# Kernel optimization log

Measured on AMD Instinct MI355X. Metric: run time of the kernel, lower is better.

## Reference

```python
import jax, jax.numpy as jnp
import numpy as np

B, S, P, D, H = 2, 4096, 1024, 1024, 16  # batch, byte seq, patches, d_model, heads


def setup_inputs() -> dict:
    key = jax.random.key(0)
    ks = jax.random.split(key, 8)
    init = 0.02
    queries = jax.random.normal(ks[0], (B, S, D), dtype=jnp.float32)
    patch_representations = jax.random.normal(ks[1], (B, P, D), dtype=jnp.float32)
    patch_boundaries = jax.random.randint(ks[2], (B, S), 0, 2, dtype=jnp.int32)
    wq = jax.random.normal(ks[3], (D, D), dtype=jnp.float32) * init
    wk = jax.random.normal(ks[4], (D, D), dtype=jnp.float32) * init
    wv = jax.random.normal(ks[5], (D, D), dtype=jnp.float32) * init
    wo = jax.random.normal(ks[6], (D, D), dtype=jnp.float32) * init
    bq = jnp.zeros((D,), jnp.float32)
    bk = jnp.zeros((D,), jnp.float32)
    bv = jnp.zeros((D,), jnp.float32)
    bo = jnp.zeros((D,), jnp.float32)
    return {"queries": queries, "patch_representations": patch_representations,
            "patch_boundaries": patch_boundaries,
            "wq": wq, "wk": wk, "wv": wv, "wo": wo,
            "bq": bq, "bk": bk, "bv": bv, "bo": bo}


def reference(queries, patch_representations, patch_boundaries,
              wq, wk, wv, wo, bq, bk, bv, bo):
    b, s, d = queries.shape
    p = patch_representations.shape[1]
    h = H
    dh = d // h
    scale = 1.0 / jnp.sqrt(jnp.asarray(dh, queries.dtype))

    # in-projections (torch Linear: x @ W.T + b)
    q = (queries @ wq.T + bq).reshape(b, s, h, dh)
    k = (patch_representations @ wk.T + bk).reshape(b, p, h, dh)
    v = (patch_representations @ wv.T + bv).reshape(b, p, h, dh)

    # scores: [b, h, s, p]
    scores = jnp.einsum('bqhd,bkhd->bhqk', q, k) * scale

    # data-dependent patch-boundary mask: byte t may attend to patch j iff j <= cumsum(boundaries)[t]
    patch_idx = jnp.cumsum(patch_boundaries, axis=1)          # [b, s]
    mask = jnp.arange(p)[None, None, :] > patch_idx[:, :, None]  # [b, s, p], True = masked
    scores = jnp.where(mask[:, None, :, :], jnp.finfo(scores.dtype).min, scores)

    attn = jax.nn.softmax(scores, axis=-1)                    # dropout inactive (eval)
    out = jnp.einsum('bhqk,bkhd->bqhd', attn, v).reshape(b, s, d)
    return out @ wo.T + bo
```

## Files before the change

kernel.cpp:

```cpp
#include <hip/hip_runtime.h>


#define B_ 2
#define S_ 4096
#define P_ 1024
#define D_ 1024
#define H_ 16
#define DH_ 64

#define NCONV 14336

typedef __attribute__((ext_vector_type(8))) short short8;
typedef __attribute__((ext_vector_type(4))) float f32x4;

#define KSCALE 0.18033688011112042f

static __device__ __forceinline__ unsigned short f2bf(float f) {
    unsigned int u = __float_as_uint(f);
    u += 0x7FFFu + ((u >> 16) & 1u);
    return (unsigned short)(u >> 16);
}

static __device__ __forceinline__ void gll16(const unsigned short* g,
                                             const unsigned short* l) {
    __builtin_amdgcn_global_load_lds(
        (const __attribute__((address_space(1))) unsigned int*)g,
        (__attribute__((address_space(3))) unsigned int*)l,
        16, 0, 0);
}

__global__ __launch_bounds__(256) void xattn_convert_all(
    const float* __restrict__ queries, const float* __restrict__ patches,
    const float* __restrict__ wq, const float* __restrict__ wk,
    const float* __restrict__ wv, const float* __restrict__ wo,
    unsigned short* __restrict__ qb, unsigned short* __restrict__ pb,
    unsigned short* __restrict__ wqb, unsigned short* __restrict__ wkb,
    unsigned short* __restrict__ wvb, unsigned short* __restrict__ wob,
    const int* __restrict__ bounds, int* __restrict__ pidx) {
    if (blockIdx.x >= NCONV) {
        __shared__ int sdata[256];
        int b = blockIdx.x - NCONV;
        int t = threadIdx.x;
        const int* src = bounds + b * S_ + t * 16;
        int vals[16];
        int run = 0;
#pragma unroll
        for (int i = 0; i < 16; ++i) { run += src[i]; vals[i] = run; }
        sdata[t] = run;
        __syncthreads();
        for (int off = 1; off < 256; off <<= 1) {
            int v = (t >= off) ? sdata[t - off] : 0;
            __syncthreads();
            sdata[t] += v;
            __syncthreads();
        }
        int prefix = (t > 0) ? sdata[t - 1] : 0;
        int* dst = pidx + b * S_ + t * 16;
#pragma unroll
        for (int i = 0; i < 16; ++i) dst[i] = prefix + vals[i];
        return;
    }
    const int NQ = (B_ * S_ * D_) / 4;
    const int NP = (B_ * P_ * D_) / 4;
    const int NW = (D_ * D_) / 4;
    int i = blockIdx.x * 256 + threadIdx.x;
    const float* src;
    unsigned short* dst;
    int j;
    if (i < NQ) { src = queries; dst = qb; j = i; }
    else if (i < NQ + NP) { src = patches; dst = pb; j = i - NQ; }
    else {
        int k = i - NQ - NP;
        int wsel = k >> 18;
        j = k & (NW - 1);
        if (wsel == 0) { src = wq; dst = wqb; }
        else if (wsel == 1) { src = wk; dst = wkb; }
        else if (wsel == 2) { src = wv; dst = wvb; }
        else { src = wo; dst = wob; }
    }
    float4 v = ((const float4*)src)[j];
    ushort4 o;
    o.x = f2bf(v.x); o.y = f2bf(v.y); o.z = f2bf(v.z); o.w = f2bf(v.w);
    ((ushort4*)dst)[j] = o;
}

__global__ __launch_bounds__(256) void xattn_gemm_qkv(
    const unsigned short* __restrict__ qb, const unsigned short* __restrict__ pb,
    const unsigned short* __restrict__ wqb, const unsigned short* __restrict__ wkb,
    const unsigned short* __restrict__ wvb,
    const float* __restrict__ bq, const float* __restrict__ bk,
    const float* __restrict__ bv,
    unsigned short* __restrict__ Qout, unsigned short* __restrict__ Kout,
    unsigned short* __restrict__ Vout) {
    const int K = 1024, N = 1024;
    const int z = blockIdx.z;
    if (z > 0 && blockIdx.y >= 16) return;
    const unsigned short* A = (z == 0) ? qb : pb;
    const unsigned short* W = (z == 0) ? wqb : ((z == 1) ? wkb : wvb);
    const float* bias = (z == 0) ? bq : ((z == 1) ? bk : bv);

    __shared__ unsigned short As[128 * 32];
    __shared__ unsigned short Bs[128 * 32];

    const int m0 = blockIdx.y * 128;
    const int n0 = blockIdx.x * 128;
    const int t = threadIdx.x;
    const int w = t >> 6;
    const int l = t & 63;
    const int fr = l & 15, fq = l >> 4;
    const int wr = w >> 1, wc = w & 1;

    const int r0s = t >> 2;
    const int cs = (t & 3) * 8;
    const unsigned short* Ap0 = A + (size_t)(m0 + r0s) * K + cs;
    const unsigned short* Ap1 = A + (size_t)(m0 + 64 + r0s) * K + cs;
    const unsigned short* Wp0 = W + (size_t)(n0 + r0s) * K + cs;
    const unsigned short* Wp1 = W + (size_t)(n0 + 64 + r0s) * K + cs;
    const unsigned short* lA0 = &As[(w * 64) * 8];
    const unsigned short* lA1 = &As[(256 + w * 64) * 8];
    const unsigned short* lB0 = &Bs[(w * 64) * 8];
    const unsigned short* lB1 = &Bs[(256 + w * 64) * 8];

    f32x4 acc[4][4];
#pragma unroll
    for (int i = 0; i < 4; ++i)
#pragma unroll
        for (int j = 0; j < 4; ++j) acc[i][j] = (f32x4){0.f, 0.f, 0.f, 0.f};

    for (int k0 = 0; k0 < K; k0 += 32) {
        gll16(Ap0 + k0, lA0);
        gll16(Ap1 + k0, lA1);
        gll16(Wp0 + k0, lB0);
        gll16(Wp1 + k0, lB1);
        __syncthreads();
        short8 af[4], bf[4];
#pragma unroll
        for (int i = 0; i < 4; ++i)
            af[i] = *(const short8*)&As[(wr * 64 + i * 16 + fr) * 32 + fq * 8];
#pragma unroll
        for (int j = 0; j < 4; ++j)
            bf[j] = *(const short8*)&Bs[(wc * 64 + j * 16 + fr) * 32 + fq * 8];
#pragma unroll
        for (int i = 0; i < 4; ++i)
#pragma unroll
            for (int j = 0; j < 4; ++j)
                acc[i][j] = __builtin_amdgcn_mfma_f32_16x16x32_bf16(af[i], bf[j], acc[i][j], 0, 0, 0);
        __syncthreads();
    }

#pragma unroll
    for (int j = 0; j < 4; ++j) {
        int n = n0 + wc * 64 + j * 16 + fr;
        float bvv = bias[n];
#pragma unroll
        for (int i = 0; i < 4; ++i) {
            int mbase = m0 + wr * 64 + i * 16 + fq * 4;
#pragma unroll
            for (int r = 0; r < 4; ++r) {
                float val = acc[i][j][r] + bvv;
                int m = mbase + r;
                if (z == 0) {
                    Qout[(size_t)m * N + n] = f2bf(val * KSCALE);
                } else if (z == 1) {
                    Kout[(size_t)m * N + n] = f2bf(val);
                } else {
                    int bb = m >> 10, c = m & (P_ - 1);
                    int hh = n >> 6, d = n & 63;
                    Vout[(((size_t)(bb * H_ + hh)) * 64 + d) * P_ + c] = f2bf(val);
                }
            }
        }
    }
}

__global__ __launch_bounds__(256) void xattn_gemm_o(
    const unsigned short* __restrict__ A,
    const unsigned short* __restrict__ W,
    const float* __restrict__ bias,
    float* __restrict__ Cout) {
    const int K = 1024, N = 1024;
    __shared__ unsigned short As[128 * 32];
    __shared__ unsigned short Bs[128 * 32];

    const int m0 = blockIdx.y * 128;
    const int n0 = blockIdx.x * 128;
    const int t = threadIdx.x;
    const int w = t >> 6;
    const int l = t & 63;
    const int fr = l & 15, fq = l >> 4;
    const int wr = w >> 1, wc = w & 1;

    const int r0s = t >> 2;
    const int cs = (t & 3) * 8;
    const unsigned short* Ap0 = A + (size_t)(m0 + r0s) * K + cs;
    const unsigned short* Ap1 = A + (size_t)(m0 + 64 + r0s) * K + cs;
    const unsigned short* Wp0 = W + (size_t)(n0 + r0s) * K + cs;
    const unsigned short* Wp1 = W + (size_t)(n0 + 64 + r0s) * K + cs;
    const unsigned short* lA0 = &As[(w * 64) * 8];
    const unsigned short* lA1 = &As[(256 + w * 64) * 8];
    const unsigned short* lB0 = &Bs[(w * 64) * 8];
    const unsigned short* lB1 = &Bs[(256 + w * 64) * 8];

    f32x4 acc[4][4];
#pragma unroll
    for (int i = 0; i < 4; ++i)
#pragma unroll
        for (int j = 0; j < 4; ++j) acc[i][j] = (f32x4){0.f, 0.f, 0.f, 0.f};

    for (int k0 = 0; k0 < K; k0 += 32) {
        gll16(Ap0 + k0, lA0);
        gll16(Ap1 + k0, lA1);
        gll16(Wp0 + k0, lB0);
        gll16(Wp1 + k0, lB1);
        __syncthreads();
        short8 af[4], bf[4];
#pragma unroll
        for (int i = 0; i < 4; ++i)
            af[i] = *(const short8*)&As[(wr * 64 + i * 16 + fr) * 32 + fq * 8];
#pragma unroll
        for (int j = 0; j < 4; ++j)
            bf[j] = *(const short8*)&Bs[(wc * 64 + j * 16 + fr) * 32 + fq * 8];
#pragma unroll
        for (int i = 0; i < 4; ++i)
#pragma unroll
            for (int j = 0; j < 4; ++j)
                acc[i][j] = __builtin_amdgcn_mfma_f32_16x16x32_bf16(af[i], bf[j], acc[i][j], 0, 0, 0);
        __syncthreads();
    }

#pragma unroll
    for (int j = 0; j < 4; ++j) {
        int n = n0 + wc * 64 + j * 16 + fr;
        float bvv = bias[n];
#pragma unroll
        for (int i = 0; i < 4; ++i) {
            int mbase = m0 + wr * 64 + i * 16 + fq * 4;
#pragma unroll
            for (int r = 0; r < 4; ++r)
                Cout[(size_t)(mbase + r) * N + n] = acc[i][j][r] + bvv;
        }
    }
}

__global__ __launch_bounds__(256) void xattn_attn_mfma(
    const unsigned short* __restrict__ Qb,
    const unsigned short* __restrict__ Kb,
    const unsigned short* __restrict__ Vtb,
    const int* __restrict__ pidx,
    unsigned short* __restrict__ Ob) {
    __shared__ unsigned short Ks[64 * 72];
    __shared__ unsigned short Vs[64 * 72];
    __shared__ unsigned short Ps[64 * 72];

    const int q0 = (63 - blockIdx.x) * 64;
    const int h = blockIdx.y;
    const int b = blockIdx.z;
    const int t = threadIdx.x;
    const int w = t >> 6, l = t & 63;
    const int fr = l & 15, fq = l >> 4;

    const unsigned short* qrow =
        Qb + (size_t)(b * S_ + q0 + w * 16 + fr) * D_ + h * DH_ + fq * 8;
    short8 qf0 = *(const short8*)qrow;
    short8 qf1 = *(const short8*)(qrow + 32);

    int prow[4];
#pragma unroll
    for (int r = 0; r < 4; ++r)
        prow[r] = pidx[b * S_ + q0 + w * 16 + fq * 4 + r];
    const int limit = pidx[b * S_ + q0 + 63];
    const int ntiles = (min(limit, P_ - 1) + 64) >> 6;
    const int nfull = (pidx[b * S_ + q0] + 1) >> 6;

    float lsum[4] = {0.f, 0.f, 0.f, 0.f};
    f32x4 oacc[4];
#pragma unroll
    for (int nt = 0; nt < 4; ++nt) oacc[nt] = (f32x4){0.f, 0.f, 0.f, 0.f};

    const int srow = t >> 3, sseg = t & 7;
    const unsigned short* kbase = Kb + (size_t)(b * P_) * D_ + h * DH_;
    const unsigned short* vbase = Vtb + (size_t)(b * H_ + h) * 64 * P_;
    unsigned short* ksa = &Ks[srow * 72 + sseg * 8];
    unsigned short* ksb = &Ks[(srow + 32) * 72 + sseg * 8];
    unsigned short* vsa = &Vs[srow * 72 + sseg * 8];
    unsigned short* vsb = &Vs[(srow + 32) * 72 + sseg * 8];

    uint4 rk0 = *(const uint4*)(kbase + (size_t)srow * D_ + sseg * 8);
    uint4 rk1 = *(const uint4*)(kbase + (size_t)(srow + 32) * D_ + sseg * 8);
    uint4 rv0 = *(const uint4*)(vbase + (size_t)srow * P_ + sseg * 8);
    uint4 rv1 = *(const uint4*)(vbase + (size_t)(srow + 32) * P_ + sseg * 8);
    *(uint4*)ksa = rk0;
    *(uint4*)ksb = rk1;
    *(uint4*)vsa = rv0;
    *(uint4*)vsb = rv1;
    __syncthreads();

    for (int kt = 0; kt < ntiles; ++kt) {
        const int c0 = kt * 64;
        const int c0n = min(c0 + 64, P_ - 64);
        rk0 = *(const uint4*)(kbase + (size_t)(c0n + srow) * D_ + sseg * 8);
        rk1 = *(const uint4*)(kbase + (size_t)(c0n + srow + 32) * D_ + sseg * 8);
        rv0 = *(const uint4*)(vbase + (size_t)srow * P_ + c0n + sseg * 8);
        rv1 = *(const uint4*)(vbase + (size_t)(srow + 32) * P_ + c0n + sseg * 8);

        const int maskme = (kt >= nfull);
#pragma unroll
        for (int nt = 0; nt < 4; ++nt) {
            short8 kf0 = *(const short8*)&Ks[(nt * 16 + fr) * 72 + fq * 8];
            short8 kf1 = *(const short8*)&Ks[(nt * 16 + fr) * 72 + 32 + fq * 8];
            const int col = c0 + nt * 16 + fr;
            f32x4 a = (f32x4){0.f, 0.f, 0.f, 0.f};
            a = __builtin_amdgcn_mfma_f32_16x16x32_bf16(qf0, kf0, a, 0, 0, 0);
            a = __builtin_amdgcn_mfma_f32_16x16x32_bf16(qf1, kf1, a, 0, 0, 0);
#pragma unroll
            for (int r = 0; r < 4; ++r) {
                float p = exp2f(a[r]);
                if (maskme) p = (col > prow[r]) ? 0.f : p;
                lsum[r] += p;
                Ps[(w * 16 + fq * 4 + r) * 72 + nt * 16 + fr] = f2bf(p);
            }
        }
        short8 pf0 = *(const short8*)&Ps[(w * 16 + fr) * 72 + fq * 8];
        short8 pf1 = *(const short8*)&Ps[(w * 16 + fr) * 72 + 32 + fq * 8];
#pragma unroll
        for (int nt = 0; nt < 4; ++nt) {
            short8 vf0 = *(const short8*)&Vs[(nt * 16 + fr) * 72 + fq * 8];
            short8 vf1 = *(const short8*)&Vs[(nt * 16 + fr) * 72 + 32 + fq * 8];
            oacc[nt] = __builtin_amdgcn_mfma_f32_16x16x32_bf16(pf0, vf0, oacc[nt], 0, 0, 0);
            oacc[nt] = __builtin_amdgcn_mfma_f32_16x16x32_bf16(pf1, vf1, oacc[nt], 0, 0, 0);
        }
        __syncthreads();
        *(uint4*)ksa = rk0;
        *(uint4*)ksb = rk1;
        *(uint4*)vsa = rv0;
        *(uint4*)vsb = rv1;
        __syncthreads();
    }

#pragma unroll
    for (int off = 1; off < 16; off <<= 1) {
#pragma unroll
        for (int r = 0; r < 4; ++r)
            lsum[r] += __shfl_xor(lsum[r], off);
    }
    float inv[4];
#pragma unroll
    for (int r = 0; r < 4; ++r) inv[r] = 1.0f / lsum[r];

    unsigned short* obase = Ob + (size_t)(b * S_ + q0 + w * 16) * D_ + h * DH_;
#pragma unroll
    for (int nt = 0; nt < 4; ++nt)
#pragma unroll
        for (int r = 0; r < 4; ++r)
            obase[(size_t)(fq * 4 + r) * D_ + nt * 16 + fr] =
                f2bf(oacc[nt][r] * inv[r]);
}

extern "C" void kernel_launch(void* const* d_in, const int* in_sizes, int n_in,
                              void* d_out, int out_size, void* d_ws, size_t ws_size,
                              hipStream_t stream) {
    const float* queries = (const float*)d_in[0];
    const float* patches = (const float*)d_in[1];
    const int* bounds    = (const int*)d_in[2];
    const float* wq = (const float*)d_in[3];
    const float* wk = (const float*)d_in[4];
    const float* wv = (const float*)d_in[5];
    const float* wo = (const float*)d_in[6];
    const float* bq = (const float*)d_in[7];
    const float* bk = (const float*)d_in[8];
    const float* bv = (const float*)d_in[9];
    const float* bo = (const float*)d_in[10];
    float* out = (float*)d_out;

    char* ws = (char*)d_ws;
    unsigned short* qb    = (unsigned short*)(ws + 0);
    unsigned short* pb    = (unsigned short*)(ws + 16777216);
    unsigned short* wqb   = (unsigned short*)(ws + 20971520);
    unsigned short* wkb   = (unsigned short*)(ws + 23068672);
    unsigned short* wvb   = (unsigned short*)(ws + 25165824);
    unsigned short* wob   = (unsigned short*)(ws + 27262976);
    unsigned short* Qbf   = (unsigned short*)(ws + 29360128);
    unsigned short* Kbf   = (unsigned short*)(ws + 46137344);
    unsigned short* Vtb   = (unsigned short*)(ws + 50331648);
    unsigned short* attnb = (unsigned short*)(ws + 54525952);
    int* pidx             = (int*)(ws + 71303168);

    xattn_convert_all<<<dim3(NCONV + B_), 256, 0, stream>>>(
        queries, patches, wq, wk, wv, wo, qb, pb, wqb, wkb, wvb, wob,
        bounds, pidx);
    xattn_gemm_qkv<<<dim3(8, 64, 3), 256, 0, stream>>>(
        qb, pb, wqb, wkb, wvb, bq, bk, bv, Qbf, Kbf, Vtb);
    xattn_attn_mfma<<<dim3(S_ / 64, H_, B_), 256, 0, stream>>>(
        Qbf, Kbf, Vtb, pidx, attnb);
    xattn_gemm_o<<<dim3(8, 64), 256, 0, stream>>>(attnb, wob, bo, out);
}
```

Baseline: 266.9 us.

## Permute V columns, pack P tile with perm stores, use fast exp2, drop register prefetch

The V projection epilogue now writes V columns in a permuted order within each 64-wide chunk. This lets the attention kernel store probabilities with packed 8-byte writes (built with byte-perm truncation to bf16) instead of sixteen scalar rounded stores. The exp2 call becomes the hardware builtin, and the masked and unmasked tiles use separate loops. The register double-buffered K/V prefetch is removed in favour of a plain load-then-sync per tile, which lowers register pressure but exposes global load latency. The packed store also truncates to bf16 instead of rounding.

```diff
diff --git a/kernel.cpp b/kernel.cpp
--- a/kernel.cpp
+++ b/kernel.cpp
@@ -14,6 +14,12 @@
 typedef __attribute__((ext_vector_type(4))) float f32x4;
 
 #define KSCALE 0.18033688011112042f
+
+#if __has_builtin(__builtin_amdgcn_exp2f)
+#define EXP2(x) __builtin_amdgcn_exp2f(x)
+#else
+#define EXP2(x) exp2f(x)
+#endif
 
 static __device__ __forceinline__ unsigned short f2bf(float f) {
     unsigned int u = __float_as_uint(f);
@@ -166,7 +172,9 @@
                 } else {
                     int bb = m >> 10, c = m & (P_ - 1);
                     int hh = n >> 6, d = n & 63;
-                    Vout[(((size_t)(bb * H_ + hh)) * 64 + d) * P_ + c] = f2bf(val);
+                    int cl = c & 63;
+                    int cp = (c & 960) | (((cl & 15) << 2) | (cl >> 4));
+                    Vout[(((size_t)(bb * H_ + hh)) * 64 + d) * P_ + cp] = f2bf(val);
                 }
             }
         }
@@ -280,45 +288,62 @@
     const int srow = t >> 3, sseg = t & 7;
     const unsigned short* kbase = Kb + (size_t)(b * P_) * D_ + h * DH_;
     const unsigned short* vbase = Vtb + (size_t)(b * H_ + h) * 64 * P_;
-    unsigned short* ksa = &Ks[srow * 72 + sseg * 8];
-    unsigned short* ksb = &Ks[(srow + 32) * 72 + sseg * 8];
-    unsigned short* vsa = &Vs[srow * 72 + sseg * 8];
-    unsigned short* vsb = &Vs[(srow + 32) * 72 + sseg * 8];
-
-    uint4 rk0 = *(const uint4*)(kbase + (size_t)srow * D_ + sseg * 8);
-    uint4 rk1 = *(const uint4*)(kbase + (size_t)(srow + 32) * D_ + sseg * 8);
-    uint4 rv0 = *(const uint4*)(vbase + (size_t)srow * P_ + sseg * 8);
-    uint4 rv1 = *(const uint4*)(vbase + (size_t)(srow + 32) * P_ + sseg * 8);
-    *(uint4*)ksa = rk0;
-    *(uint4*)ksb = rk1;
-    *(uint4*)vsa = rv0;
-    *(uint4*)vsb = rv1;
-    __syncthreads();
 
     for (int kt = 0; kt < ntiles; ++kt) {
         const int c0 = kt * 64;
-        const int c0n = min(c0 + 64, P_ - 64);
-        rk0 = *(const uint4*)(kbase + (size_t)(c0n + srow) * D_ + sseg * 8);
-        rk1 = *(const uint4*)(kbase + (size_t)(c0n + srow + 32) * D_ + sseg * 8);
-        rv0 = *(const uint4*)(vbase + (size_t)srow * P_ + c0n + sseg * 8);
-        rv1 = *(const uint4*)(vbase + (size_t)(srow + 32) * P_ + c0n + sseg * 8);
+        __syncthreads();
+        *(uint4*)&Ks[srow * 72 + sseg * 8] =
+            *(const uint4*)(kbase + (size_t)(c0 + srow) * D_ + sseg * 8);
+        *(uint4*)&Ks[(srow + 32) * 72 + sseg * 8] =
+            *(const uint4*)(kbase + (size_t)(c0 + srow + 32) * D_ + sseg * 8);
+        *(uint4*)&Vs[srow * 72 + sseg * 8] =
+            *(const uint4*)(vbase + (size_t)srow * P_ + c0 + sseg * 8);
+        *(uint4*)&Vs[(srow + 32) * 72 + sseg * 8] =
+            *(const uint4*)(vbase + (size_t)(srow + 32) * P_ + c0 + sseg * 8);
+        __syncthreads();
 
         const int maskme = (kt >= nfull);
+        f32x4 s[4];
 #pragma unroll
         for (int nt = 0; nt < 4; ++nt) {
             short8 kf0 = *(const short8*)&Ks[(nt * 16 + fr) * 72 + fq * 8];
             short8 kf1 = *(const short8*)&Ks[(nt * 16 + fr) * 72 + 32 + fq * 8];
-            const int col = c0 + nt * 16 + fr;
             f32x4 a = (f32x4){0.f, 0.f, 0.f, 0.f};
             a = __builtin_amdgcn_mfma_f32_16x16x32_bf16(qf0, kf0, a, 0, 0, 0);
             a = __builtin_amdgcn_mfma_f32_16x16x32_bf16(qf1, kf1, a, 0, 0, 0);
-#pragma unroll
-            for (int r = 0; r < 4; ++r) {
-                float p = exp2f(a[r]);
-                if (maskme) p = (col > prow[r]) ? 0.f : p;
-                lsum[r] += p;
-                Ps[(w * 16 + fq * 4 + r) * 72 + nt * 16 + fr] = f2bf(p);
+            s[nt] = a;
+        }
+        if (maskme) {
+#pragma unroll
+            for (int nt = 0; nt < 4; ++nt) {
+                const int col = c0 + nt * 16 + fr;
+#pragma unroll
+                for (int r = 0; r < 4; ++r) {
+                    float p = EXP2(s[nt][r]);
+                    p = (col > prow[r]) ? 0.f : p;
+                    s[nt][r] = p;
+                    lsum[r] += p;
+                }
             }
+        } else {
+#pragma unroll
+            for (int nt = 0; nt < 4; ++nt) {
+#pragma unroll
+                for (int r = 0; r < 4; ++r) {
+                    float p = EXP2(s[nt][r]);
+                    s[nt][r] = p;
+                    lsum[r] += p;
+                }
+            }
+        }
+#pragma unroll
+        for (int r = 0; r < 4; ++r) {
+            uint2 pk;
+            pk.x = __builtin_amdgcn_perm(__float_as_uint(s[1][r]),
+                                         __float_as_uint(s[0][r]), 0x07060302u);
+            pk.y = __builtin_amdgcn_perm(__float_as_uint(s[3][r]),
+                                         __float_as_uint(s[2][r]), 0x07060302u);
+            *(uint2*)&Ps[(w * 16 + fq * 4 + r) * 72 + fr * 4] = pk;
         }
         short8 pf0 = *(const short8*)&Ps[(w * 16 + fr) * 72 + fq * 8];
         short8 pf1 = *(const short8*)&Ps[(w * 16 + fr) * 72 + 32 + fq * 8];
@@ -329,12 +354,6 @@
             oacc[nt] = __builtin_amdgcn_mfma_f32_16x16x32_bf16(pf0, vf0, oacc[nt], 0, 0, 0);
             oacc[nt] = __builtin_amdgcn_mfma_f32_16x16x32_bf16(pf1, vf1, oacc[nt], 0, 0, 0);
         }
-        __syncthreads();
-        *(uint4*)ksa = rk0;
-        *(uint4*)ksb = rk1;
-        *(uint4*)vsa = rv0;
-        *(uint4*)vsb = rv1;
-        __syncthreads();
     }
 
 #pragma unroll
```

Result: faster. 245.4 us (-8.1%).
